# Performance work log

Hardware: AMD Instinct MI355X
Metric: run time of the kernel (lower is better)

## Reference

```python
import jax, jax.numpy as jnp
import numpy as np

T, B, H = 2048, 32, 1024


def setup_inputs() -> dict:
    key = jax.random.key(0)
    k1, k2, k3 = jax.random.split(key, 3)
    t_input = jax.random.normal(k1, (T, B, H), dtype=jnp.float32)
    h0 = jax.random.normal(k2, (B, H), dtype=jnp.float32)
    # weight_hh ~ U(0, 1) per reset_parameters default
    weight_hh = jax.random.uniform(k3, (H,), dtype=jnp.float32)
    return {"t_input": t_input, "h0": h0, "weight_hh": weight_hh}


def reference(t_input, h0, weight_hh):
    # h_t = relu(x_t + whh * h_{t-1}); per-channel recurrent scan over time.
    def step(h, x):
        h_new = jax.nn.relu(x + weight_hh * h)  # (B, H)
        return h_new, h_new

    _, out = jax.lax.scan(step, h0, t_input)  # out: (T, B, H)
    return out
```

## Files before the change

### kernel.cpp

```cpp
#include <hip/hip_runtime.h>


#define T_STEPS 2048
#define B_DIM   32
#define H_DIM   1024
#define BH      (B_DIM * H_DIM)
#define BH4     (BH / 4)
#define NCHUNK  32
#define CLEN    (T_STEPS / NCHUNK)
#define PF      8

typedef float f4 __attribute__((ext_vector_type(4)));

__device__ __forceinline__ f4 step_relu(const f4 w, const f4 h, const f4 x) {
    f4 r;
    r.x = fmaxf(fmaf(w.x, h.x, x.x), 0.f);
    r.y = fmaxf(fmaf(w.y, h.y, x.y), 0.f);
    r.z = fmaxf(fmaf(w.z, h.z, x.z), 0.f);
    r.w = fmaxf(fmaf(w.w, h.w, x.w), 0.f);
    return r;
}

__device__ __forceinline__ f4 step_lin(const f4 w, const f4 a, const f4 x) {
    f4 r;
    r.x = fmaf(w.x, a.x, x.x);
    r.y = fmaf(w.y, a.y, x.y);
    r.z = fmaf(w.z, a.z, x.z);
    r.w = fmaf(w.w, a.w, x.w);
    return r;
}

__global__ __launch_bounds__(256, 4)
void indrnn_pass1(const f4* __restrict__ x, const f4* __restrict__ h0,
                  const f4* __restrict__ w,
                  f4* __restrict__ m_out, f4* __restrict__ a_out)
{
    const int tid = blockIdx.x * 256 + threadIdx.x;
    const int c   = tid >> 13;
    const int c4  = tid & (BH4 - 1);
    const f4 wv = w[c4 & (H_DIM / 4 - 1)];

    f4 m, a;
    a.x = a.y = a.z = a.w = 0.f;
    if (c == 0) {
        m = h0[c4];
    } else {
        m.x = m.y = m.z = m.w = 0.f;
    }

    const f4* xp = x + (size_t)c * CLEN * BH4 + c4;

    f4 buf[PF];
#pragma unroll
    for (int i = 0; i < PF; ++i)
        buf[i] = xp[(size_t)i * BH4];

    int t0 = 0;
    for (; t0 + PF < CLEN; t0 += PF) {
        f4 nxt[PF];
#pragma unroll
        for (int i = 0; i < PF; ++i)
            nxt[i] = xp[(size_t)(t0 + PF + i) * BH4];
#pragma unroll
        for (int i = 0; i < PF; ++i) {
            m = step_relu(wv, m, buf[i]);
            a = step_lin(wv, a, buf[i]);
        }
#pragma unroll
        for (int i = 0; i < PF; ++i) buf[i] = nxt[i];
    }
#pragma unroll
    for (int i = 0; i < PF; ++i) {
        m = step_relu(wv, m, buf[i]);
        a = step_lin(wv, a, buf[i]);
    }

    m_out[(size_t)c * BH4 + c4] = m;
    a_out[(size_t)c * BH4 + c4] = a;
}

__global__ __launch_bounds__(256, 1)
void indrnn_pass2(const float* __restrict__ h0, const float* __restrict__ w,
                  const float* __restrict__ m, const float* __restrict__ a,
                  float* __restrict__ hstart)
{
    const int ch = blockIdx.x * 256 + threadIdx.x;
    const float wv = w[ch & (H_DIM - 1)];
    float b = wv;
#pragma unroll
    for (int i = 0; i < 6; ++i) b *= b;

    float mv[NCHUNK], av[NCHUNK];
#pragma unroll
    for (int cc = 0; cc < NCHUNK; ++cc) {
        mv[cc] = m[cc * BH + ch];
        av[cc] = a[cc * BH + ch];
    }

    float h = h0[ch];
    hstart[ch] = h;
    h = mv[0];
    hstart[BH + ch] = h;
#pragma unroll
    for (int cc = 2; cc < NCHUNK; ++cc) {
        h = fmaxf(fmaf(b, h, av[cc - 1]), mv[cc - 1]);
        hstart[cc * BH + ch] = h;
    }
}

__global__ __launch_bounds__(256, 4)
void indrnn_pass3(const f4* __restrict__ x, const f4* __restrict__ hstart,
                  const f4* __restrict__ w, f4* __restrict__ out)
{
    const int tid = blockIdx.x * 256 + threadIdx.x;
    const int c   = tid >> 13;
    const int c4  = tid & (BH4 - 1);
    const f4 wv = w[c4 & (H_DIM / 4 - 1)];

    f4 h = hstart[(size_t)c * BH4 + c4];

    const f4* xp = x + (size_t)c * CLEN * BH4 + c4;
    f4* op = out + (size_t)c * CLEN * BH4 + c4;

    f4 buf[PF];
#pragma unroll
    for (int i = 0; i < PF; ++i)
        buf[i] = xp[(size_t)i * BH4];

    int t0 = 0;
    for (; t0 + PF < CLEN; t0 += PF) {
        f4 nxt[PF];
#pragma unroll
        for (int i = 0; i < PF; ++i)
            nxt[i] = xp[(size_t)(t0 + PF + i) * BH4];
#pragma unroll
        for (int i = 0; i < PF; ++i) {
            h = step_relu(wv, h, buf[i]);
            op[(size_t)(t0 + i) * BH4] = h;
        }
#pragma unroll
        for (int i = 0; i < PF; ++i) buf[i] = nxt[i];
    }
#pragma unroll
    for (int i = 0; i < PF; ++i) {
        h = step_relu(wv, h, buf[i]);
        op[(size_t)(t0 + i) * BH4] = h;
    }
}

extern "C" void kernel_launch(void* const* d_in, const int* in_sizes, int n_in,
                              void* d_out, int out_size, void* d_ws, size_t ws_size,
                              hipStream_t stream) {
    const f4* x  = (const f4*)d_in[0];
    const f4* h0 = (const f4*)d_in[1];
    const f4* w  = (const f4*)d_in[2];
    f4* out = (f4*)d_out;

    float* m  = (float*)d_ws;
    float* a  = m + (size_t)NCHUNK * BH;
    float* hs = a + (size_t)NCHUNK * BH;

    indrnn_pass1<<<(NCHUNK * BH4) / 256, 256, 0, stream>>>(
        x, h0, w, (f4*)m, (f4*)a);
    indrnn_pass2<<<BH / 256, 256, 0, stream>>>(
        (const float*)h0, (const float*)w, m, a, hs);
    indrnn_pass3<<<(NCHUNK * BH4) / 256, 256, 0, stream>>>(
        x, (const f4*)hs, w, out);
}
```

Baseline: 514.0 us.

## Fuse three-pass chunked scan into single kernel with decoupled lookback

Replaces the summarize / carry-propagate / rescan pipeline with one kernel. Each block computes its chunk's (m, a) summary, publishes it with a release flag, then spins on the flags of all earlier chunks for its channel group. It combines their summaries to get its starting state and immediately rescans its own chunk to write outputs. This removes the serial pass2 launch and the hstart round-trip, and rereads x soon after the first read, so it may still be cache-resident. In exchange, each block re-folds up to 31 prior summaries and depends on all blocks being co-resident to avoid a spin deadlock.

```diff
diff --git a/kernel.cpp b/kernel.cpp
--- a/kernel.cpp
+++ b/kernel.cpp
@@ -8,6 +8,7 @@
 #define BH4     (BH / 4)
 #define NCHUNK  32
 #define CLEN    (T_STEPS / NCHUNK)
+#define GRPS    (BH4 / 256)
 #define PF      8
 
 typedef float f4 __attribute__((ext_vector_type(4)));
@@ -30,37 +31,46 @@
     return r;
 }
 
+__global__ void zero_flags(unsigned* __restrict__ f) {
+    f[blockIdx.x * 256 + threadIdx.x] = 0u;
+}
+
 __global__ __launch_bounds__(256, 4)
-void indrnn_pass1(const f4* __restrict__ x, const f4* __restrict__ h0,
-                  const f4* __restrict__ w,
-                  f4* __restrict__ m_out, f4* __restrict__ a_out)
+void indrnn_lookback(const f4* __restrict__ x, const f4* __restrict__ h0,
+                     const f4* __restrict__ w, f4* __restrict__ out,
+                     f4* __restrict__ m_ws, f4* __restrict__ a_ws,
+                     unsigned* __restrict__ flags)
 {
-    const int tid = blockIdx.x * 256 + threadIdx.x;
-    const int c   = tid >> 13;
-    const int c4  = tid & (BH4 - 1);
-    const f4 wv = w[c4 & (H_DIM / 4 - 1)];
+    const int bid = blockIdx.x;
+    const int c   = bid >> 5;
+    const int g   = bid & 31;
+    const int tid = threadIdx.x;
+    const int q   = (g << 8) + tid;
 
-    f4 m, a;
-    a.x = a.y = a.z = a.w = 0.f;
-    if (c == 0) {
-        m = h0[c4];
-    } else {
-        m.x = m.y = m.z = m.w = 0.f;
+    const f4 wv = w[tid];
+
+    f4 b4 = wv;
+#pragma unroll
+    for (int i = 0; i < 6; ++i) {
+        b4.x *= b4.x; b4.y *= b4.y; b4.z *= b4.z; b4.w *= b4.w;
     }
 
-    const f4* xp = x + (size_t)c * CLEN * BH4 + c4;
+    const f4* xp = x + (size_t)c * CLEN * BH4 + q;
+
+    f4 m, a, h0v;
+    a.x = a.y = a.z = a.w = 0.f;
+    if (c == 0) { h0v = h0[q]; m = h0v; }
+    else        { m.x = m.y = m.z = m.w = 0.f; }
 
     f4 buf[PF];
 #pragma unroll
-    for (int i = 0; i < PF; ++i)
-        buf[i] = xp[(size_t)i * BH4];
+    for (int i = 0; i < PF; ++i) buf[i] = xp[(size_t)i * BH4];
 
     int t0 = 0;
     for (; t0 + PF < CLEN; t0 += PF) {
         f4 nxt[PF];
 #pragma unroll
-        for (int i = 0; i < PF; ++i)
-            nxt[i] = xp[(size_t)(t0 + PF + i) * BH4];
+        for (int i = 0; i < PF; ++i) nxt[i] = xp[(size_t)(t0 + PF + i) * BH4];
 #pragma unroll
         for (int i = 0; i < PF; ++i) {
             m = step_relu(wv, m, buf[i]);
@@ -75,64 +85,50 @@
         a = step_lin(wv, a, buf[i]);
     }
 
-    m_out[(size_t)c * BH4 + c4] = m;
-    a_out[(size_t)c * BH4 + c4] = a;
-}
+    m_ws[(size_t)c * BH4 + q] = m;
+    a_ws[(size_t)c * BH4 + q] = a;
+    __syncthreads();
+    if (tid == 0)
+        __hip_atomic_store(&flags[bid], 1u, __ATOMIC_RELEASE,
+                           __HIP_MEMORY_SCOPE_AGENT);
 
-__global__ __launch_bounds__(256, 1)
-void indrnn_pass2(const float* __restrict__ h0, const float* __restrict__ w,
-                  const float* __restrict__ m, const float* __restrict__ a,
-                  float* __restrict__ hstart)
-{
-    const int ch = blockIdx.x * 256 + threadIdx.x;
-    const float wv = w[ch & (H_DIM - 1)];
-    float b = wv;
-#pragma unroll
-    for (int i = 0; i < 6; ++i) b *= b;
+    f4 v;
+    if (c == 0) {
+        v = h0v;
+    } else {
+        if (tid < c) {
+            const unsigned* fp = &flags[(tid << 5) | g];
+            while (__hip_atomic_load(fp, __ATOMIC_ACQUIRE,
+                                     __HIP_MEMORY_SCOPE_AGENT) == 0u)
+                __builtin_amdgcn_s_sleep(1);
+        }
+        __syncthreads();
 
-    float mv[NCHUNK], av[NCHUNK];
-#pragma unroll
-    for (int cc = 0; cc < NCHUNK; ++cc) {
-        mv[cc] = m[cc * BH + ch];
-        av[cc] = a[cc * BH + ch];
+        const f4* mp = m_ws + q;
+        const f4* ap = a_ws + q;
+        v = mp[0];
+#pragma unroll 4
+        for (int j = 1; j < c; ++j) {
+            const f4 mj = mp[(size_t)j * BH4];
+            const f4 aj = ap[(size_t)j * BH4];
+            v.x = fmaxf(fmaf(b4.x, v.x, aj.x), mj.x);
+            v.y = fmaxf(fmaf(b4.y, v.y, aj.y), mj.y);
+            v.z = fmaxf(fmaf(b4.z, v.z, aj.z), mj.z);
+            v.w = fmaxf(fmaf(b4.w, v.w, aj.w), mj.w);
+        }
     }
 
-    float h = h0[ch];
-    hstart[ch] = h;
-    h = mv[0];
-    hstart[BH + ch] = h;
+    f4 h = v;
+    f4* op = out + (size_t)c * CLEN * BH4 + q;
+
 #pragma unroll
-    for (int cc = 2; cc < NCHUNK; ++cc) {
-        h = fmaxf(fmaf(b, h, av[cc - 1]), mv[cc - 1]);
-        hstart[cc * BH + ch] = h;
-    }
-}
+    for (int i = 0; i < PF; ++i) buf[i] = xp[(size_t)i * BH4];
 
-__global__ __launch_bounds__(256, 4)
-void indrnn_pass3(const f4* __restrict__ x, const f4* __restrict__ hstart,
-                  const f4* __restrict__ w, f4* __restrict__ out)
-{
-    const int tid = blockIdx.x * 256 + threadIdx.x;
-    const int c   = tid >> 13;
-    const int c4  = tid & (BH4 - 1);
-    const f4 wv = w[c4 & (H_DIM / 4 - 1)];
-
-    f4 h = hstart[(size_t)c * BH4 + c4];
-
-    const f4* xp = x + (size_t)c * CLEN * BH4 + c4;
-    f4* op = out + (size_t)c * CLEN * BH4 + c4;
-
-    f4 buf[PF];
-#pragma unroll
-    for (int i = 0; i < PF; ++i)
-        buf[i] = xp[(size_t)i * BH4];
-
-    int t0 = 0;
+    t0 = 0;
     for (; t0 + PF < CLEN; t0 += PF) {
         f4 nxt[PF];
 #pragma unroll
-        for (int i = 0; i < PF; ++i)
-            nxt[i] = xp[(size_t)(t0 + PF + i) * BH4];
+        for (int i = 0; i < PF; ++i) nxt[i] = xp[(size_t)(t0 + PF + i) * BH4];
 #pragma unroll
         for (int i = 0; i < PF; ++i) {
             h = step_relu(wv, h, buf[i]);
@@ -156,14 +152,11 @@
     const f4* w  = (const f4*)d_in[2];
     f4* out = (f4*)d_out;
 
-    float* m  = (float*)d_ws;
-    float* a  = m + (size_t)NCHUNK * BH;
-    float* hs = a + (size_t)NCHUNK * BH;
+    float* m = (float*)d_ws;
+    float* a = m + (size_t)NCHUNK * BH;
+    unsigned* flags = (unsigned*)(a + (size_t)NCHUNK * BH);
 
-    indrnn_pass1<<<(NCHUNK * BH4) / 256, 256, 0, stream>>>(
-        x, h0, w, (f4*)m, (f4*)a);
-    indrnn_pass2<<<BH / 256, 256, 0, stream>>>(
-        (const float*)h0, (const float*)w, m, a, hs);
-    indrnn_pass3<<<(NCHUNK * BH4) / 256, 256, 0, stream>>>(
-        x, (const f4*)hs, w, out);
+    zero_flags<<<(NCHUNK * GRPS) / 256, 256, 0, stream>>>(flags);
+    indrnn_lookback<<<NCHUNK * GRPS, 256, 0, stream>>>(
+        x, h0, w, out, (f4*)m, (f4*)a, flags);
 }
```

After: 555.2 us. +8.0%, slower.
